# Kernel optimization log

Measured on AMD Instinct MI355X. Metric: run time of the kernel, lower is better.

## Reference

```python
import jax, jax.numpy as jnp
import numpy as np

T = 100000
M = 32
PI_CONST = 3.1415926  # matches the constant used in the original source


def setup_inputs() -> dict:
    key = jax.random.key(0)
    k1, k2, k3, k4, k5, k6 = jax.random.split(key, 6)
    obs_2_T = jax.random.normal(k1, (T,), dtype=jnp.float32)
    obs_1_T_1 = jax.random.normal(k2, (T,), dtype=jnp.float32)
    mean = jax.random.normal(k3, (M,), dtype=jnp.float32)
    # variances must be positive
    var = jax.random.uniform(k4, (M,), dtype=jnp.float32) + jnp.float32(0.5)
    bate = jnp.float32(0.85)
    # pi: valid initial distribution; aij: row-stochastic transition matrix
    pi = jax.nn.softmax(jax.random.normal(k5, (M,), dtype=jnp.float32))
    aij = jax.nn.softmax(jax.random.normal(k6, (M, M), dtype=jnp.float32), axis=-1)
    return {"obs_2_T": obs_2_T, "obs_1_T_1": obs_1_T_1, "mean": mean,
            "var": var, "bate": bate, "pi": pi, "aij": aij}


def reference(obs_2_T, obs_1_T_1, mean, var, bate, pi, aij):
    # Eta[i, j, t] = exp(-(obs2[t] - (mean[j] + bate*(obs1[t] - mean[i]))) / (2*var[j]))
    #               / sqrt(2*pi*var[j])
    # (NOTE: faithful to the source, which does NOT square the residual.)
    inv2v = 1.0 / (2.0 * var)                      # (m,)
    norm = 1.0 / jnp.sqrt(2.0 * PI_CONST * var)    # (m,)
    # diff: (m_i, m_j, T)
    diff = obs_2_T[None, None, :] - (mean[None, :, None]
                                     + bate * (obs_1_T_1[None, None, :] - mean[:, None, None]))
    Eta = jnp.exp(-diff * inv2v[None, :, None]) * norm[None, :, None]  # (m, m, T)
    Eta_t = jnp.moveaxis(Eta, -1, 0)  # (T, m, m)

    # Normalized forward recursion:
    # t=0: num[i,j] = Eta[i,j,0] * pi[i] * aij[i,j]
    # t>0: num[i,j] = Eta[i,j,t] * Epsilon[t-1,i] * aij[i,j]
    # Gamma[t] = num / sum(num);  Epsilon[t,j] = sum_i Gamma[t,i,j]
    def step(eps_prev, eta):  # eps_prev: (m,), eta: (m, m)
        num = eta * eps_prev[:, None] * aij
        g = num / jnp.sum(num)
        return jnp.sum(g, axis=0), g

    _, Gamma = jax.lax.scan(step, pi, Eta_t)  # Gamma: (T, m, m)

    # loss = sum_t <Gamma[t], Eta[:, :, t]>
    loss = jnp.sum(Gamma * Eta_t)
    return loss
```

## Files before the change

### kernel.cpp

```cpp
#include <hip/hip_runtime.h>

constexpr int TN   = 100000;
constexpr int NCH  = 4000;
constexpr int CLEN = 25;
constexpr int WARM = 24;
constexpr int WPB  = 4;
constexpr int NBLK = NCH / WPB;
constexpr int MAXS = WARM + CLEN;

constexpr float LOG2E = 1.4426950408889634f;
constexpr float PI_F  = 3.1415926f;

#define ROR(src, N) __int_as_float(__builtin_amdgcn_mov_dpp( \
    __float_as_int(src), 0x120 + (N), 0xF, 0xF, false))

#define ROTS(SRC, R)                                                          \
  float R##1 = ROR(SRC, 1),  R##2 = ROR(SRC, 2),  R##3 = ROR(SRC, 3),         \
        R##4 = ROR(SRC, 4),  R##5 = ROR(SRC, 5),  R##6 = ROR(SRC, 6),         \
        R##7 = ROR(SRC, 7),  R##8 = ROR(SRC, 8),  R##9 = ROR(SRC, 9),         \
        R##10 = ROR(SRC,10), R##11 = ROR(SRC,11), R##12 = ROR(SRC,12),        \
        R##13 = ROR(SRC,13), R##14 = ROR(SRC,14), R##15 = ROR(SRC,15);

#define DOT16(Wr, SRC, R, dd)                                                 \
  float dd;                                                                   \
  { float q0 = Wr[0]*(SRC)  + Wr[4]*R##4;                                     \
    float q1 = Wr[1]*R##1   + Wr[5]*R##5;                                     \
    float q2 = Wr[2]*R##2   + Wr[6]*R##6;                                     \
    float q3 = Wr[3]*R##3   + Wr[7]*R##7;                                     \
    q0 += Wr[8]*R##8;   q1 += Wr[9]*R##9;                                     \
    q2 += Wr[10]*R##10; q3 += Wr[11]*R##11;                                   \
    q0 += Wr[12]*R##12; q1 += Wr[13]*R##13;                                   \
    q2 += Wr[14]*R##14; q3 += Wr[15]*R##15;                                   \
    dd = (q0 + q1) + (q2 + q3); }

#define RING16(v) { v += ROR(v,1); v += ROR(v,2); v += ROR(v,4); v += ROR(v,8); }

__global__ __launch_bounds__(256, 4) void k_main(
    const float* __restrict__ obs2, const float* __restrict__ obs1,
    const float* __restrict__ mean_p, const float* __restrict__ var_p,
    const float* __restrict__ bate_p, const float* __restrict__ pi_p,
    const float* __restrict__ aij, float* __restrict__ lossbuf)
{
  const int w = threadIdx.x >> 6, lane = threadIdx.x & 63;
  const int wv = blockIdx.x * WPB + w;
  const int i  = lane & 15;
  const int h  = lane >> 5;
  const int j  = lane & 31;
  const int kb = h * 16;

  __shared__ __align__(16) float Wsh[2][32][32];
  __shared__ float cts[WPB][MAXS + 3];

  {
    const int tid = threadIdx.x;
    const int jj = tid & 31, ig = tid >> 5;
    float vjq  = var_p[jj];
    float i2vq = 0.5f / vjq;
    float norm = rsqrtf(2.0f * PI_F * vjq);
    float Aj   = norm * expf(mean_p[jj] * i2vq);
    float bate = bate_p[0];
#pragma unroll
    for (int m = 0; m < 4; ++m) {
      int ii = ig * 4 + m;
      float Bij = expf(-bate * mean_p[ii] * i2vq);
      float wq = aij[ii * 32 + jj] * Aj * Bij;
      Wsh[0][ii][jj] = wq;
      Wsh[1][ii][jj] = wq * Aj * Bij;
    }
  }

  float vj  = var_p[j];
  float i2v = 0.5f / vj;
  float s_  = i2v;
#pragma unroll
  for (int o = 1; o < 32; o <<= 1) s_ += __shfl_xor(s_, o);
  const float i2vl = i2v * LOG2E;
  const float i2vc = (i2v - s_ * 0.03125f) * LOG2E;

  const int t0 = wv * CLEN;
  const int tw = (t0 > WARM) ? (t0 - WARM) : 0;
  const int n  = t0 + CLEN - tw;
  const int warmsteps = t0 - tw;
  {
    float bate = bate_p[0];
    for (int l = lane; l < n; l += 64)
      cts[w][l] = obs2[tw + l] - bate * obs1[tw + l];
  }
  __syncthreads();

  int dird;
  { int p = __builtin_amdgcn_mov_dpp(i, 0x121, 0xF, 0xF, false);
    dird = (p - i) & 15; }

  float Wr[16], Vr[16];
#pragma unroll
  for (int N = 0; N < 16; ++N) {
    int kk = (i + N * dird) & 15;
    Wr[N] = Wsh[0][kb + kk][j];
    Vr[N] = Wsh[1][kb + kk][j];
  }

  const bool takeT = (((lane >> 4) & 1) ^ h) != 0;

  float y = (tw == 0) ? pi_p[j] : 0.03125f;
  float t = __shfl_xor(y, 16);
  float ysrc = takeT ? t : y;

  for (int s = 0; s < warmsteps; ++s) {
    float ct = cts[w][s];
    float u  = exp2f(-ct * i2vc);
    ROTS(ysrc, a)
    DOT16(Wr, ysrc, a, pW)
    float dot = pW + __shfl_xor(pW, 32);
    y = u * dot;
    if ((s & 3) == 3)
      y *= __builtin_amdgcn_rcpf(__int_as_float(
             __builtin_amdgcn_readfirstlane(__float_as_int(y))));
    t = __shfl_xor(y, 16);
    ysrc = takeT ? t : y;
  }
  float lossacc = 0.f;
#pragma unroll 5
  for (int q = 0; q < CLEN; ++q) {
    float ct = cts[w][warmsteps + q];
    float u  = exp2f(-ct * i2vl);
    ROTS(ysrc, a)
    DOT16(Wr, ysrc, a, pW)
    DOT16(Vr, ysrc, a, pV)
    float dotW = pW + __shfl_xor(pW, 32);
    float dotV = pV + __shfl_xor(pV, 32);
    float numj = u * dotW;
    float n2j  = (u * u) * dotV;
    y = numj;
    if ((q & 3) == 3)
      y *= __builtin_amdgcn_rcpf(__int_as_float(
             __builtin_amdgcn_readfirstlane(__float_as_int(y))));
    t = __shfl_xor(y, 16);
    ysrc = takeT ? t : y;
    float red = h ? n2j : numj;
    RING16(red)
    red += __shfl_xor(red, 16);
    float cross = __shfl_xor(red, 32);
    float S  = h ? cross : red;
    float N2 = h ? red   : cross;
    lossacc += N2 * __builtin_amdgcn_rcpf(S);
  }
  if (lane == 0) lossbuf[wv] = lossacc;
}

__global__ __launch_bounds__(256) void k_finish(const float* __restrict__ lb,
                                                float* __restrict__ out)
{
  const int tid = threadIdx.x;
  float v = 0.f;
  for (int l = tid; l < NCH; l += 256) v += lb[l];
#pragma unroll
  for (int o = 1; o < 64; o <<= 1) v += __shfl_xor(v, o);
  __shared__ float part[4];
  if ((tid & 63) == 0) part[tid >> 6] = v;
  __syncthreads();
  if (tid == 0) out[0] = part[0] + part[1] + part[2] + part[3];
}

extern "C" void kernel_launch(void* const* d_in, const int* in_sizes, int n_in,
                              void* d_out, int out_size, void* d_ws, size_t ws_size,
                              hipStream_t stream)
{
  (void)in_sizes; (void)n_in; (void)ws_size; (void)out_size;
  const float* obs2 = (const float*)d_in[0];
  const float* obs1 = (const float*)d_in[1];
  const float* mean = (const float*)d_in[2];
  const float* var  = (const float*)d_in[3];
  const float* bate = (const float*)d_in[4];
  const float* pi   = (const float*)d_in[5];
  const float* aij  = (const float*)d_in[6];
  float* lb  = (float*)d_ws;
  float* out = (float*)d_out;

  k_main  <<<NBLK, 256, 0, stream>>>(obs2, obs1, mean, var, bate, pi, aij, lb);
  k_finish<<<1,    256, 0, stream>>>(lb, out);
}
```

Baseline: 91.93 us.

## Pack dot products into float2 ops, shorten chunks, relax renormalization cadence

Measured after the change: 93.93 us. 2.2% more time.

```diff
diff --git a/kernel.cpp b/kernel.cpp
--- a/kernel.cpp
+++ b/kernel.cpp
@@ -1,9 +1,9 @@
 #include <hip/hip_runtime.h>
 
 constexpr int TN   = 100000;
-constexpr int NCH  = 4000;
-constexpr int CLEN = 25;
-constexpr int WARM = 24;
+constexpr int NCH  = 5000;
+constexpr int CLEN = 20;
+constexpr int WARM = 16;
 constexpr int WPB  = 4;
 constexpr int NBLK = NCH / WPB;
 constexpr int MAXS = WARM + CLEN;
@@ -11,31 +11,28 @@
 constexpr float LOG2E = 1.4426950408889634f;
 constexpr float PI_F  = 3.1415926f;
 
+typedef float v2f __attribute__((ext_vector_type(2)));
+
 #define ROR(src, N) __int_as_float(__builtin_amdgcn_mov_dpp( \
     __float_as_int(src), 0x120 + (N), 0xF, 0xF, false))
 
-#define ROTS(SRC, R)                                                          \
-  float R##1 = ROR(SRC, 1),  R##2 = ROR(SRC, 2),  R##3 = ROR(SRC, 3),         \
-        R##4 = ROR(SRC, 4),  R##5 = ROR(SRC, 5),  R##6 = ROR(SRC, 6),         \
-        R##7 = ROR(SRC, 7),  R##8 = ROR(SRC, 8),  R##9 = ROR(SRC, 9),         \
-        R##10 = ROR(SRC,10), R##11 = ROR(SRC,11), R##12 = ROR(SRC,12),        \
-        R##13 = ROR(SRC,13), R##14 = ROR(SRC,14), R##15 = ROR(SRC,15);
-
-#define DOT16(Wr, SRC, R, dd)                                                 \
-  float dd;                                                                   \
-  { float q0 = Wr[0]*(SRC)  + Wr[4]*R##4;                                     \
-    float q1 = Wr[1]*R##1   + Wr[5]*R##5;                                     \
-    float q2 = Wr[2]*R##2   + Wr[6]*R##6;                                     \
-    float q3 = Wr[3]*R##3   + Wr[7]*R##7;                                     \
-    q0 += Wr[8]*R##8;   q1 += Wr[9]*R##9;                                     \
-    q2 += Wr[10]*R##10; q3 += Wr[11]*R##11;                                   \
-    q0 += Wr[12]*R##12; q1 += Wr[13]*R##13;                                   \
-    q2 += Wr[14]*R##14; q3 += Wr[15]*R##15;                                   \
-    dd = (q0 + q1) + (q2 + q3); }
-
 #define RING16(v) { v += ROR(v,1); v += ROR(v,2); v += ROR(v,4); v += ROR(v,8); }
 
-__global__ __launch_bounds__(256, 4) void k_main(
+#define ROTPAIRS(SRC, P)                                                      \
+  v2f P[8];                                                                   \
+  { P[0] = (v2f){SRC,        ROR(SRC,1)};  P[1] = (v2f){ROR(SRC,2),  ROR(SRC,3)};  \
+    P[2] = (v2f){ROR(SRC,4), ROR(SRC,5)};  P[3] = (v2f){ROR(SRC,6),  ROR(SRC,7)};  \
+    P[4] = (v2f){ROR(SRC,8), ROR(SRC,9)};  P[5] = (v2f){ROR(SRC,10), ROR(SRC,11)}; \
+    P[6] = (v2f){ROR(SRC,12),ROR(SRC,13)}; P[7] = (v2f){ROR(SRC,14), ROR(SRC,15)}; }
+
+#define PKDOT(Wp, P, dd)                                                      \
+  float dd;                                                                   \
+  { v2f a0 = Wp[0]*P[0], a1 = Wp[1]*P[1], a2 = Wp[2]*P[2], a3 = Wp[3]*P[3];   \
+    a0 += Wp[4]*P[4]; a1 += Wp[5]*P[5]; a2 += Wp[6]*P[6]; a3 += Wp[7]*P[7];   \
+    v2f b = (a0 + a1) + (a2 + a3);                                            \
+    dd = b.x + b.y; }
+
+__global__ __launch_bounds__(256, 5) void k_main(
     const float* __restrict__ obs2, const float* __restrict__ obs1,
     const float* __restrict__ mean_p, const float* __restrict__ var_p,
     const float* __restrict__ bate_p, const float* __restrict__ pi_p,
@@ -49,7 +46,7 @@
   const int kb = h * 16;
 
   __shared__ __align__(16) float Wsh[2][32][32];
-  __shared__ float cts[WPB][MAXS + 3];
+  __shared__ float cts[WPB][MAXS + 4];
 
   {
     const int tid = threadIdx.x;
@@ -74,8 +71,9 @@
   float s_  = i2v;
 #pragma unroll
   for (int o = 1; o < 32; o <<= 1) s_ += __shfl_xor(s_, o);
-  const float i2vl = i2v * LOG2E;
-  const float i2vc = (i2v - s_ * 0.03125f) * LOG2E;
+  const float mbar = s_ * 0.03125f;
+  const float i2vc = (i2v - mbar) * LOG2E;
+  const float Mc   = mbar * LOG2E;
 
   const int t0 = wv * CLEN;
   const int tw = (t0 > WARM) ? (t0 - WARM) : 0;
@@ -92,12 +90,13 @@
   { int p = __builtin_amdgcn_mov_dpp(i, 0x121, 0xF, 0xF, false);
     dird = (p - i) & 15; }
 
-  float Wr[16], Vr[16];
+  v2f Wp[8], Vp[8];
 #pragma unroll
-  for (int N = 0; N < 16; ++N) {
-    int kk = (i + N * dird) & 15;
-    Wr[N] = Wsh[0][kb + kk][j];
-    Vr[N] = Wsh[1][kb + kk][j];
+  for (int N = 0; N < 8; ++N) {
+    int k0 = (i + (2 * N)     * dird) & 15;
+    int k1 = (i + (2 * N + 1) * dird) & 15;
+    Wp[N] = (v2f){Wsh[0][kb + k0][j], Wsh[0][kb + k1][j]};
+    Vp[N] = (v2f){Wsh[1][kb + k0][j], Wsh[1][kb + k1][j]};
   }
 
   const bool takeT = (((lane >> 4) & 1) ^ h) != 0;
@@ -109,30 +108,31 @@
   for (int s = 0; s < warmsteps; ++s) {
     float ct = cts[w][s];
     float u  = exp2f(-ct * i2vc);
-    ROTS(ysrc, a)
-    DOT16(Wr, ysrc, a, pW)
+    ROTPAIRS(ysrc, P)
+    PKDOT(Wp, P, pW)
     float dot = pW + __shfl_xor(pW, 32);
     y = u * dot;
-    if ((s & 3) == 3)
+    if ((s & 7) == 7)
       y *= __builtin_amdgcn_rcpf(__int_as_float(
              __builtin_amdgcn_readfirstlane(__float_as_int(y))));
     t = __shfl_xor(y, 16);
     ysrc = takeT ? t : y;
   }
   float lossacc = 0.f;
-#pragma unroll 5
+#pragma unroll 4
   for (int q = 0; q < CLEN; ++q) {
-    float ct = cts[w][warmsteps + q];
-    float u  = exp2f(-ct * i2vl);
-    ROTS(ysrc, a)
-    DOT16(Wr, ysrc, a, pW)
-    DOT16(Vr, ysrc, a, pV)
+    float ct   = cts[w][warmsteps + q];
+    float u    = exp2f(-ct * i2vc);
+    float corr = exp2f(-ct * Mc);
+    ROTPAIRS(ysrc, P)
+    PKDOT(Wp, P, pW)
+    PKDOT(Vp, P, pV)
     float dotW = pW + __shfl_xor(pW, 32);
     float dotV = pV + __shfl_xor(pV, 32);
     float numj = u * dotW;
     float n2j  = (u * u) * dotV;
     y = numj;
-    if ((q & 3) == 3)
+    if ((q & 7) == 7)
       y *= __builtin_amdgcn_rcpf(__int_as_float(
              __builtin_amdgcn_readfirstlane(__float_as_int(y))));
     t = __shfl_xor(y, 16);
@@ -143,7 +143,7 @@
     float cross = __shfl_xor(red, 32);
     float S  = h ? cross : red;
     float N2 = h ? red   : cross;
-    lossacc += N2 * __builtin_amdgcn_rcpf(S);
+    lossacc += corr * N2 * __builtin_amdgcn_rcpf(S);
   }
   if (lane == 0) lossbuf[wv] = lossacc;
 }
```
